# Optimization experiments

Hardware: AMD Instinct MI355X
Metric: run time of the kernel (lower is better)

## Reference

```python
import jax, jax.numpy as jnp
import numpy as np

L, N, E, H = 4096, 1, 1024, 16
DH = E // H
SCALE = DH ** -0.5


def setup_inputs() -> dict:
    key = jax.random.key(0)
    k1, k2, k3 = jax.random.split(key, 3)
    # xavier_uniform-ish scales for faithfulness of magnitude
    lim_qkv = (6.0 / (3 * E + E)) ** 0.5
    lim_out = (6.0 / (E + E)) ** 0.5
    x = jax.random.normal(k1, (L, N, E), dtype=jnp.float32)
    w_qkv = jax.random.uniform(k2, (3 * E, E), dtype=jnp.float32, minval=-lim_qkv, maxval=lim_qkv)
    w_out = jax.random.uniform(k3, (E, E), dtype=jnp.float32, minval=-lim_out, maxval=lim_out)
    return {"x": x, "w_qkv": w_qkv, "w_out": w_out}


def reference(x, w_qkv, w_out):
    # x: [L, N, E]
    qkv = jnp.einsum('lne,fe->lnf', x, w_qkv)          # [L, N, 3E]
    q, k, v = jnp.split(qkv, 3, axis=-1)               # each [L, N, E]

    def to_heads(t):
        # [L, N, E] -> [N*H, L, DH]
        return t.reshape(L, N * H, DH).transpose(1, 0, 2)

    q = to_heads(q) * SCALE
    k = to_heads(k)
    v = to_heads(v)
    attn = jnp.einsum('bld,bmd->blm', q, k)            # [N*H, L, L]
    attn = jax.nn.softmax(attn, axis=-1)
    out = jnp.einsum('blm,bmd->bld', attn, v)          # [N*H, L, DH]
    out = out.transpose(1, 0, 2).reshape(L, N, E)
    return jnp.einsum('lne,fe->lnf', out, w_out)       # [L, N, E]
```

## Files before the change

kernel.cpp:

```cpp
#include <hip/hip_runtime.h>
#include <hip/hip_bf16.h>
#include <stdint.h>

#define L_SEQ 4096
#define EMB   1024
#define NHEAD 16
#define DHEAD 64

#define SM_SCALE 0.18033688011112042f
#define SM_FIXED_MAX 12.0f

typedef __attribute__((ext_vector_type(8))) short short8;
typedef __attribute__((ext_vector_type(4))) short s16x4;
typedef __attribute__((ext_vector_type(4))) float f32x4;

struct Pack8 { f32x4 lo, hi; };

__device__ inline short f2bf(float f) {
  union { float f; unsigned u; } c; c.f = f;
  unsigned r = (c.u + 0x7fffu + ((c.u >> 16) & 1u)) >> 16;
  return (short)(unsigned short)r;
}
__device__ inline unsigned fbits(float f) {
  union { float f; unsigned u; } c; c.f = f; return c.u;
}
__device__ inline unsigned pack_trunc(float f0, float f1) {
#if __has_builtin(__builtin_amdgcn_perm)
  return __builtin_amdgcn_perm(fbits(f1), fbits(f0), 0x07060302u);
#else
  return (fbits(f0) >> 16) | (fbits(f1) & 0xffff0000u);
#endif
}

#if __has_builtin(__builtin_amdgcn_exp2f)
#define EXP2F(x) __builtin_amdgcn_exp2f(x)
#else
#define EXP2F(x) exp2f(x)
#endif

__device__ inline void pl16swap(unsigned &x, unsigned &y) {
#if __has_builtin(__builtin_amdgcn_permlane16_swap)
  auto r = __builtin_amdgcn_permlane16_swap(x, y, false, false);
  x = r[0]; y = r[1];
#else
  asm volatile("v_permlane16_swap_b32 %0, %1" : "+v"(x), "+v"(y));
#endif
}

__device__ inline short8 mk8(unsigned d0, unsigned d1, unsigned d2, unsigned d3) {
  union { unsigned u[4]; short8 s; } c;
  c.u[0] = d0; c.u[1] = d1; c.u[2] = d2; c.u[3] = d3;
  return c.s;
}

template<bool F32>
__device__ inline auto ld8(const void* p, size_t off) {
  if constexpr (F32) {
    const float* f = (const float*)p + off;
    Pack8 r; r.lo = *(const f32x4*)f; r.hi = *(const f32x4*)(f + 4);
    return r;
  } else {
    return *(const short8*)((const short*)p + off);
  }
}
__device__ inline short8 cvt8(Pack8 r) {
  short8 o;
#pragma unroll
  for (int j = 0; j < 4; ++j) { o[j] = f2bf(r.lo[j]); o[4 + j] = f2bf(r.hi[j]); }
  return o;
}
__device__ inline short8 cvt8(short8 r) { return r; }

#define MFMA16(a, b, c) __builtin_amdgcn_mfma_f32_16x16x32_bf16(a, b, c, 0, 0, 0)
#define FZERO ((f32x4){0.f, 0.f, 0.f, 0.f})

__device__ inline void stage16(const void* g, void* l) {
  __builtin_amdgcn_global_load_lds(
      (const __attribute__((address_space(1))) void*)g,
      (__attribute__((address_space(3))) void*)l, 16, 0, 0);
}

__global__ __launch_bounds__(256)
void conv_kernel(const float* __restrict__ in, short* __restrict__ out, int n) {
  int i = (blockIdx.x * 256 + threadIdx.x) * 8;
  if (i >= n) return;
  Pack8 r; r.lo = *(const f32x4*)(in + i); r.hi = *(const f32x4*)(in + i + 4);
  *(short8*)(out + i) = cvt8(r);
}

__global__ __launch_bounds__(256, 3)
void gemm_qkv_dma(const short* __restrict__ A, const short* __restrict__ B,
                  short* __restrict__ qb, short* __restrict__ kb,
                  short* __restrict__ vt) {
  __shared__ __align__(16) short At[128 * 32];
  __shared__ __align__(16) short Bt[128 * 32];

  const int tid  = threadIdx.x;
  const int lane = tid & 63;
  const int wave = tid >> 6;
  const int quad = lane >> 4;
  const int l15  = lane & 15;
  const int q8   = quad << 3;

  const int bm  = (blockIdx.x / 24) << 7;
  const int bn  = (blockIdx.x % 24) << 7;
  const int wr  = wave >> 1;
  const int wc  = wave & 1;

  const short* Ab = A + (size_t)bm * EMB;
  const short* Bb = B + (size_t)bn * EMB;

  f32x4 acc[4][4];
#pragma unroll
  for (int r = 0; r < 4; ++r)
#pragma unroll
    for (int c = 0; c < 4; ++c) acc[r][c] = FZERO;

  const int arow = (wr * 64 + l15) * 32 + q8;
  const int brow = (wc * 64 + l15) * 32 + q8;
  const int wbase = tid & ~63;

  for (int kt = 0; kt < 32; ++kt) {
    __syncthreads();
    const int k0 = kt << 5;
#pragma unroll
    for (int j = 0; j < 2; ++j) {
      const int s = j * 256 + tid;
      const int row = s >> 2, qc = (s & 3) << 3;
      stage16(Ab + (size_t)row * EMB + k0 + qc,
              At + (size_t)(j * 256 + wbase) * 8);
      stage16(Bb + (size_t)row * EMB + k0 + qc,
              Bt + (size_t)(j * 256 + wbase) * 8);
    }
    __syncthreads();

    short8 af[4], bf[4];
#pragma unroll
    for (int r = 0; r < 4; ++r) af[r] = *(const short8*)(At + arow + r * 512);
#pragma unroll
    for (int c = 0; c < 4; ++c) bf[c] = *(const short8*)(Bt + brow + c * 512);
#pragma unroll
    for (int r = 0; r < 4; ++r)
#pragma unroll
      for (int c = 0; c < 4; ++c)
        acc[r][c] = MFMA16(af[r], bf[c], acc[r][c]);
  }

  if (bn < 2048) {
    short* dst = (bn < 1024) ? qb : kb;
    const int bcol = (bn < 1024) ? bn : bn - 1024;
    const float cs = (bn < 1024) ? SM_SCALE : 1.0f;
#pragma unroll
    for (int r = 0; r < 4; ++r)
#pragma unroll
      for (int c = 0; c < 4; ++c) {
        const int col = bcol + wc * 64 + c * 16 + l15;
#pragma unroll
        for (int reg = 0; reg < 4; ++reg) {
          const int row = bm + wr * 64 + r * 16 + quad * 4 + reg;
          dst[(size_t)row * EMB + col] = f2bf(acc[r][c][reg] * cs);
        }
      }
  } else {
    const int bcol = bn - 2048;
#pragma unroll
    for (int r = 0; r < 4; ++r)
#pragma unroll
      for (int c = 0; c < 4; ++c) {
        const int col  = bcol + wc * 64 + c * 16 + l15;
        const int rowb = bm + wr * 64 + r * 16 + quad * 4;
        s16x4 pk;
#pragma unroll
        for (int reg = 0; reg < 4; ++reg) pk[reg] = f2bf(acc[r][c][reg]);
        *(s16x4*)(vt + (size_t)col * L_SEQ + rowb) = pk;
      }
  }
}

__global__ __launch_bounds__(256, 3)
void gemm_qkv_f32(const short* __restrict__ A, const float* __restrict__ B,
                  short* __restrict__ qb, short* __restrict__ kb,
                  short* __restrict__ vt) {
  __shared__ __align__(16) short At[128 * 40];
  __shared__ __align__(16) short Bt[128 * 40];

  const int tid  = threadIdx.x;
  const int lane = tid & 63;
  const int wave = tid >> 6;
  const int quad = lane >> 4;
  const int l15  = lane & 15;
  const int q8   = quad << 3;

  const int bm  = (blockIdx.x / 24) << 7;
  const int bn  = (blockIdx.x % 24) << 7;
  const int wr  = wave >> 1;
  const int wc  = wave & 1;

  const int s0 = tid, s1 = tid + 256;
  const int ar0 = s0 >> 2, ac0 = (s0 & 3) << 3;
  const int ar1 = s1 >> 2, ac1 = (s1 & 3) << 3;

  const size_t aoff0 = (size_t)(bm + ar0) * EMB + ac0;
  const size_t aoff1 = (size_t)(bm + ar1) * EMB + ac1;
  const size_t boff0 = (size_t)(bn + ar0) * EMB + ac0;
  const size_t boff1 = (size_t)(bn + ar1) * EMB + ac1;

  f32x4 acc[4][4];
#pragma unroll
  for (int r = 0; r < 4; ++r)
#pragma unroll
    for (int c = 0; c < 4; ++c) acc[r][c] = FZERO;

  short8 ga0 = *(const short8*)(A + aoff0);
  short8 ga1 = *(const short8*)(A + aoff1);
  Pack8  gb0 = ld8<true>(B, boff0);
  Pack8  gb1 = ld8<true>(B, boff1);

  const int arow = (wr * 64 + l15) * 40 + q8;
  const int brow = (wc * 64 + l15) * 40 + q8;

  for (int kt = 0; kt < 32; ++kt) {
    __syncthreads();
    *(short8*)(At + ar0 * 40 + ac0) = ga0;
    *(short8*)(At + ar1 * 40 + ac1) = ga1;
    *(short8*)(Bt + ar0 * 40 + ac0) = cvt8(gb0);
    *(short8*)(Bt + ar1 * 40 + ac1) = cvt8(gb1);
    __syncthreads();

    if (kt + 1 < 32) {
      const size_t k0 = (size_t)(kt + 1) << 5;
      ga0 = *(const short8*)(A + aoff0 + k0);
      ga1 = *(const short8*)(A + aoff1 + k0);
      gb0 = ld8<true>(B, boff0 + k0);
      gb1 = ld8<true>(B, boff1 + k0);
    }

    short8 af[4], bf[4];
#pragma unroll
    for (int r = 0; r < 4; ++r) af[r] = *(const short8*)(At + arow + r * 640);
#pragma unroll
    for (int c = 0; c < 4; ++c) bf[c] = *(const short8*)(Bt + brow + c * 640);
#pragma unroll
    for (int r = 0; r < 4; ++r)
#pragma unroll
      for (int c = 0; c < 4; ++c)
        acc[r][c] = MFMA16(af[r], bf[c], acc[r][c]);
  }

  if (bn < 2048) {
    short* dst = (bn < 1024) ? qb : kb;
    const int bcol = (bn < 1024) ? bn : bn - 1024;
    const float cs = (bn < 1024) ? SM_SCALE : 1.0f;
#pragma unroll
    for (int r = 0; r < 4; ++r)
#pragma unroll
      for (int c = 0; c < 4; ++c) {
        const int col = bcol + wc * 64 + c * 16 + l15;
#pragma unroll
        for (int reg = 0; reg < 4; ++reg) {
          const int row = bm + wr * 64 + r * 16 + quad * 4 + reg;
          dst[(size_t)row * EMB + col] = f2bf(acc[r][c][reg] * cs);
        }
      }
  } else {
    const int bcol = bn - 2048;
#pragma unroll
    for (int r = 0; r < 4; ++r)
#pragma unroll
      for (int c = 0; c < 4; ++c) {
        const int col  = bcol + wc * 64 + c * 16 + l15;
        const int rowb = bm + wr * 64 + r * 16 + quad * 4;
        s16x4 pk;
#pragma unroll
        for (int reg = 0; reg < 4; ++reg) pk[reg] = f2bf(acc[r][c][reg]);
        *(s16x4*)(vt + (size_t)col * L_SEQ + rowb) = pk;
      }
  }
}

__global__ __launch_bounds__(256, 3)
void gemm_out_dma(const short* __restrict__ A, const short* __restrict__ B,
                  float* __restrict__ C) {
  __shared__ __align__(16) short At[128 * 32];
  __shared__ __align__(16) short Bt[64 * 32];

  const int tid  = threadIdx.x;
  const int lane = tid & 63;
  const int wave = tid >> 6;
  const int quad = lane >> 4;
  const int l15  = lane & 15;
  const int q8   = quad << 3;

  const int bm  = (blockIdx.x >> 4) << 7;
  const int bn  = (blockIdx.x & 15) << 6;
  const int wr  = wave >> 1;
  const int wc  = wave & 1;

  const short* Ab = A + (size_t)bm * EMB;
  const short* Bb = B + (size_t)bn * EMB;

  f32x4 acc[4][2];
#pragma unroll
  for (int r = 0; r < 4; ++r)
#pragma unroll
    for (int c = 0; c < 2; ++c) acc[r][c] = FZERO;

  const int arow = (wr * 64 + l15) * 32 + q8;
  const int brow = (wc * 32 + l15) * 32 + q8;
  const int wbase = tid & ~63;

  for (int kt = 0; kt < 32; ++kt) {
    __syncthreads();
    const int k0 = kt << 5;
#pragma unroll
    for (int j = 0; j < 2; ++j) {
      const int s = j * 256 + tid;
      const int row = s >> 2, qc = (s & 3) << 3;
      stage16(Ab + (size_t)row * EMB + k0 + qc,
              At + (size_t)(j * 256 + wbase) * 8);
    }
    {
      const int row = tid >> 2, qc = (tid & 3) << 3;
      stage16(Bb + (size_t)row * EMB + k0 + qc, Bt + (size_t)wbase * 8);
    }
    __syncthreads();

    short8 af[4], bf[2];
#pragma unroll
    for (int r = 0; r < 4; ++r) af[r] = *(const short8*)(At + arow + r * 512);
#pragma unroll
    for (int c = 0; c < 2; ++c) bf[c] = *(const short8*)(Bt + brow + c * 512);
#pragma unroll
    for (int r = 0; r < 4; ++r)
#pragma unroll
      for (int c = 0; c < 2; ++c)
        acc[r][c] = MFMA16(af[r], bf[c], acc[r][c]);
  }

#pragma unroll
  for (int r = 0; r < 4; ++r) {
#pragma unroll
    for (int c = 0; c < 2; ++c) {
      const int col = bn + wc * 32 + c * 16 + l15;
#pragma unroll
      for (int reg = 0; reg < 4; ++reg) {
        const int row = bm + wr * 64 + r * 16 + quad * 4 + reg;
        C[(size_t)row * EMB + col] = acc[r][c][reg];
      }
    }
  }
}

__global__ __launch_bounds__(256, 2)
void attn_kernel(short* __restrict__ qo, const short* __restrict__ kbuf,
                 const short* __restrict__ vtbuf) {
  __shared__ __align__(16) short Kt[2][64 * 72];
  __shared__ __align__(16) short Vt[2][64 * 72];

  const int tid  = threadIdx.x;
  const int lane = tid & 63;
  const int w    = tid >> 6;
  const int quad = lane >> 4;
  const int l15  = lane & 15;
  const int q8   = quad << 3;
  const int vb   = ((quad & 1) << 4) | ((quad >> 1) << 3);

  const int h    = blockIdx.x >> 5;
  const int qblk = blockIdx.x & 31;
  const int hcol = h * 64;

  const int srow = tid >> 3;
  const int sc8  = (tid & 7) << 3;

  short8 qf[2][2];
#pragma unroll
  for (int g = 0; g < 2; ++g) {
    const short* qp = qo + (size_t)(qblk * 128 + w * 32 + g * 16 + l15) * EMB + hcol;
    qf[g][0] = *(const short8*)(qp + q8);
    qf[g][1] = *(const short8*)(qp + 32 + q8);
  }

  const short8 vone = {0x3F80, 0x3F80, 0x3F80, 0x3F80,
                       0x3F80, 0x3F80, 0x3F80, 0x3F80};

  f32x4 o[2][4];
#pragma unroll
  for (int g = 0; g < 2; ++g)
#pragma unroll
    for (int f = 0; f < 4; ++f) o[g][f] = FZERO;
  f32x4 l_c[2] = {FZERO, FZERO};

  const size_t koff0 = (size_t)srow * EMB + hcol + sc8;
  const size_t voff0 = (size_t)(hcol + srow) * L_SEQ + sc8;
  const size_t krr = (size_t)32 * EMB;
  const size_t vrr = (size_t)32 * L_SEQ;

  short8 gk0 = *(const short8*)(kbuf + koff0);
  short8 gk1 = *(const short8*)(kbuf + koff0 + krr);
  short8 gv0 = *(const short8*)(vtbuf + voff0);
  short8 gv1 = *(const short8*)(vtbuf + voff0 + vrr);

  for (int t = 0; t < 64; ++t) {
    short* const ktb = &Kt[t & 1][0];
    short* const vtb = &Vt[t & 1][0];

    *(short8*)(ktb + srow * 72 + sc8) = gk0;
    *(short8*)(ktb + (srow + 32) * 72 + sc8) = gk1;
    *(short8*)(vtb + srow * 72 + sc8) = gv0;
    *(short8*)(vtb + (srow + 32) * 72 + sc8) = gv1;
    __syncthreads();

    if (t < 63) {
      const size_t kk = (size_t)(t + 1) * 64;
      gk0 = *(const short8*)(kbuf + koff0 + kk * EMB);
      gk1 = *(const short8*)(kbuf + koff0 + krr + kk * EMB);
      gv0 = *(const short8*)(vtbuf + voff0 + kk);
      gv1 = *(const short8*)(vtbuf + voff0 + vrr + kk);
    }

    f32x4 s[2][4];
#pragma unroll
    for (int f = 0; f < 4; ++f) {
      const int krow = (f * 16 + l15) * 72;
      short8 kf0 = *(const short8*)(ktb + krow + q8);
      short8 kf1 = *(const short8*)(ktb + krow + 32 + q8);
      s[0][f] = MFMA16(kf0, qf[0][0], FZERO);
      s[0][f] = MFMA16(kf1, qf[0][1], s[0][f]);
      s[1][f] = MFMA16(kf0, qf[1][0], FZERO);
      s[1][f] = MFMA16(kf1, qf[1][1], s[1][f]);
    }

    short8 pa[2][2];
#pragma unroll
    for (int g = 0; g < 2; ++g) {
      float p[4][4];
#pragma unroll
      for (int f = 0; f < 4; ++f)
#pragma unroll
        for (int r = 0; r < 4; ++r)
          p[f][r] = EXP2F(s[g][f][r] - SM_FIXED_MAX);

      unsigned pk[4][2];
#pragma unroll
      for (int f = 0; f < 4; ++f) {
        pk[f][0] = pack_trunc(p[f][0], p[f][1]);
        pk[f][1] = pack_trunc(p[f][2], p[f][3]);
      }
      pl16swap(pk[0][0], pk[1][0]);
      pl16swap(pk[0][1], pk[1][1]);
      pl16swap(pk[2][0], pk[3][0]);
      pl16swap(pk[2][1], pk[3][1]);
      pa[g][0] = mk8(pk[0][0], pk[0][1], pk[1][0], pk[1][1]);
      pa[g][1] = mk8(pk[2][0], pk[2][1], pk[3][0], pk[3][1]);

      f32x4 rsv = MFMA16(pa[g][0], vone, FZERO);
      rsv = MFMA16(pa[g][1], vone, rsv);
#pragma unroll
      for (int r = 0; r < 4; ++r) l_c[g][r] += rsv[r];
    }

#pragma unroll
    for (int f = 0; f < 4; ++f) {
      const int vrow = (f * 16 + l15) * 72;
      short8 v0 = *(const short8*)(vtb + vrow + vb);
      short8 v1 = *(const short8*)(vtb + vrow + 32 + vb);
      o[0][f] = MFMA16(pa[0][0], v0, o[0][f]);
      o[0][f] = MFMA16(pa[0][1], v1, o[0][f]);
      o[1][f] = MFMA16(pa[1][0], v0, o[1][f]);
      o[1][f] = MFMA16(pa[1][1], v1, o[1][f]);
    }
  }

  __syncthreads();
  short* const pw = &Kt[0][0] + w * (32 * 72);
#pragma unroll
  for (int g = 0; g < 2; ++g) {
    f32x4 inv;
#pragma unroll
    for (int r = 0; r < 4; ++r) inv[r] = 1.0f / l_c[g][r];
    short* const pg = pw + g * (16 * 72);
#pragma unroll
    for (int f = 0; f < 4; ++f)
#pragma unroll
      for (int r = 0; r < 4; ++r)
        pg[(quad * 4 + r) * 72 + f * 16 + l15] = f2bf(o[g][f][r] * inv[r]);
  }

#pragma unroll
  for (int rr = 0; rr < 4; ++rr) {
    const int row = (lane >> 3) + rr * 8;
    const int c8  = (lane & 7) << 3;
    short8 gv = *(const short8*)(pw + row * 72 + c8);
    *(short8*)(qo + (size_t)(qblk * 128 + w * 32 + row) * EMB + hcol + c8) = gv;
  }
}

extern "C" void kernel_launch(void* const* d_in, const int* in_sizes, int n_in,
                              void* d_out, int out_size, void* d_ws, size_t ws_size,
                              hipStream_t stream) {
  (void)in_sizes; (void)n_in; (void)out_size;
  const float* x     = (const float*)d_in[0];
  const float* w_qkv = (const float*)d_in[1];
  const float* w_out = (const float*)d_in[2];

  short* qbuf  = (short*)d_ws;
  short* x_bf  = qbuf + (size_t)L_SEQ * EMB;
  short* wo_bf = x_bf;
  short* wq_bf = x_bf + (size_t)L_SEQ * EMB;
  short* kbuf  = (short*)d_out;
  short* vtbuf = kbuf + (size_t)L_SEQ * EMB;
  float* outp  = (float*)d_out;

  const bool big_ws = ws_size >= (size_t)24 * 1024 * 1024;

  conv_kernel<<<dim3(L_SEQ * EMB / 2048), 256, 0, stream>>>(x, x_bf, L_SEQ * EMB);
  if (big_ws)
    conv_kernel<<<dim3(3 * EMB * EMB / 2048), 256, 0, stream>>>(w_qkv, wq_bf, 3 * EMB * EMB);

  if (big_ws)
    gemm_qkv_dma<<<dim3(768), 256, 0, stream>>>(x_bf, wq_bf, qbuf, kbuf, vtbuf);
  else
    gemm_qkv_f32<<<dim3(768), 256, 0, stream>>>(x_bf, w_qkv, qbuf, kbuf, vtbuf);

  conv_kernel<<<dim3(EMB * EMB / 2048), 256, 0, stream>>>(w_out, wo_bf, EMB * EMB);

  attn_kernel<<<dim3(NHEAD * (L_SEQ / 128)), 256, 0, stream>>>(qbuf, kbuf, vtbuf);

  gemm_out_dma<<<dim3(512), 256, 0, stream>>>(qbuf, wo_bf, outp);
}
```

Before: 217.0 us.

## Stage K/V tiles directly to LDS with XOR swizzle and raise occupancy

Replaces register-staged global loads plus LDS stores in the attention kernel with a stage16 helper that copies global memory straight into LDS (global-to-LDS loads). The padded 72-stride tiles become unpadded 64-stride tiles with an XOR column swizzle, which shrinks shared memory so launch bounds can allow 3 blocks per CU. This is meant to cut register pressure and VGPR round trips for staging and to hide latency through higher occupancy. The risk is that the async LDS writes may not be ordered correctly against the single barrier per iteration. The epilogue still indexes with the old 72 stride inside the new buffer, which is also a risk.

New measurement: 217.0 us. About the same (+0.0%).

```diff
diff --git a/kernel.cpp b/kernel.cpp
--- a/kernel.cpp
+++ b/kernel.cpp
@@ -351,11 +351,10 @@
   }
 }
 
-__global__ __launch_bounds__(256, 2)
+__global__ __launch_bounds__(256, 3)
 void attn_kernel(short* __restrict__ qo, const short* __restrict__ kbuf,
                  const short* __restrict__ vtbuf) {
-  __shared__ __align__(16) short Kt[2][64 * 72];
-  __shared__ __align__(16) short Vt[2][64 * 72];
+  __shared__ __align__(16) short SH[4][64 * 64];
 
   const int tid  = threadIdx.x;
   const int lane = tid & 63;
@@ -369,9 +368,6 @@
   const int qblk = blockIdx.x & 31;
   const int hcol = h * 64;
 
-  const int srow = tid >> 3;
-  const int sc8  = (tid & 7) << 3;
-
   short8 qf[2][2];
 #pragma unroll
   for (int g = 0; g < 2; ++g) {
@@ -390,40 +386,47 @@
     for (int f = 0; f < 4; ++f) o[g][f] = FZERO;
   f32x4 l_c[2] = {FZERO, FZERO};
 
-  const size_t koff0 = (size_t)srow * EMB + hcol + sc8;
-  const size_t voff0 = (size_t)(hcol + srow) * L_SEQ + sc8;
-  const size_t krr = (size_t)32 * EMB;
-  const size_t vrr = (size_t)32 * L_SEQ;
-
-  short8 gk0 = *(const short8*)(kbuf + koff0);
-  short8 gk1 = *(const short8*)(kbuf + koff0 + krr);
-  short8 gv0 = *(const short8*)(vtbuf + voff0);
-  short8 gv1 = *(const short8*)(vtbuf + voff0 + vrr);
+  const int r0  = tid >> 3;
+  const int lc8 = ((tid & 7) ^ (r0 & 7)) << 3;
+  const short* kp0 = kbuf + (size_t)r0 * EMB + hcol + lc8;
+  const short* kp1 = kp0 + (size_t)32 * EMB;
+  const short* vp0 = vtbuf + (size_t)(hcol + r0) * L_SEQ + lc8;
+  const short* vp1 = vp0 + (size_t)32 * L_SEQ;
+  const int d0 = (tid & ~63) * 8;
+  const int d1 = 2048 + d0;
+
+  const int sx8 = (l15 & 7) << 3;
+  const int pk0 = q8 ^ sx8, pk1 = pk0 ^ 32;
+  const int pv0 = vb ^ sx8, pv1 = pv0 ^ 32;
+
+  stage16(kp0, &SH[0][0] + d0);
+  stage16(kp1, &SH[0][0] + d1);
+  stage16(vp0, &SH[2][0] + d0);
+  stage16(vp1, &SH[2][0] + d1);
 
   for (int t = 0; t < 64; ++t) {
-    short* const ktb = &Kt[t & 1][0];
-    short* const vtb = &Vt[t & 1][0];
-
-    *(short8*)(ktb + srow * 72 + sc8) = gk0;
-    *(short8*)(ktb + (srow + 32) * 72 + sc8) = gk1;
-    *(short8*)(vtb + srow * 72 + sc8) = gv0;
-    *(short8*)(vtb + (srow + 32) * 72 + sc8) = gv1;
+    short* const ktb = &SH[t & 1][0];
+    short* const vtb = &SH[2 + (t & 1)][0];
+
     __syncthreads();
 
     if (t < 63) {
-      const size_t kk = (size_t)(t + 1) * 64;
-      gk0 = *(const short8*)(kbuf + koff0 + kk * EMB);
-      gk1 = *(const short8*)(kbuf + koff0 + krr + kk * EMB);
-      gv0 = *(const short8*)(vtbuf + voff0 + kk);
-      gv1 = *(const short8*)(vtbuf + voff0 + vrr + kk);
+      const size_t ko = (size_t)(t + 1) * 64 * EMB;
+      const size_t vo = (size_t)(t + 1) * 64;
+      short* const kd = &SH[(t + 1) & 1][0];
+      short* const vd = &SH[2 + ((t + 1) & 1)][0];
+      stage16(kp0 + ko, kd + d0);
+      stage16(kp1 + ko, kd + d1);
+      stage16(vp0 + vo, vd + d0);
+      stage16(vp1 + vo, vd + d1);
     }
 
     f32x4 s[2][4];
 #pragma unroll
     for (int f = 0; f < 4; ++f) {
-      const int krow = (f * 16 + l15) * 72;
-      short8 kf0 = *(const short8*)(ktb + krow + q8);
-      short8 kf1 = *(const short8*)(ktb + krow + 32 + q8);
+      const int krow = (f * 16 + l15) * 64;
+      short8 kf0 = *(const short8*)(ktb + krow + pk0);
+      short8 kf1 = *(const short8*)(ktb + krow + pk1);
       s[0][f] = MFMA16(kf0, qf[0][0], FZERO);
       s[0][f] = MFMA16(kf1, qf[0][1], s[0][f]);
       s[1][f] = MFMA16(kf0, qf[1][0], FZERO);
@@ -461,9 +464,9 @@
 
 #pragma unroll
     for (int f = 0; f < 4; ++f) {
-      const int vrow = (f * 16 + l15) * 72;
-      short8 v0 = *(const short8*)(vtb + vrow + vb);
-      short8 v1 = *(const short8*)(vtb + vrow + 32 + vb);
+      const int vrow = (f * 16 + l15) * 64;
+      short8 v0 = *(const short8*)(vtb + vrow + pv0);
+      short8 v1 = *(const short8*)(vtb + vrow + pv1);
       o[0][f] = MFMA16(pa[0][0], v0, o[0][f]);
       o[0][f] = MFMA16(pa[0][1], v1, o[0][f]);
       o[1][f] = MFMA16(pa[1][0], v0, o[1][f]);
@@ -472,7 +475,7 @@
   }
 
   __syncthreads();
-  short* const pw = &Kt[0][0] + w * (32 * 72);
+  short* const pw = &SH[0][0] + w * (32 * 72);
 #pragma unroll
   for (int g = 0; g < 2; ++g) {
     f32x4 inv;
```
